# Optimization experiments

Measured on AMD Instinct MI355X. Metric: run time of the kernel, lower is better.

The kernel has to match this reference:

```python
import jax, jax.numpy as jnp
import numpy as np

B, LQ, LK, D = 16, 2048, 2048, 64
TEMPERATURE = 8.0  # sqrt(d_k)


def setup_inputs() -> dict:
    key = jax.random.key(0)
    kq, kk, kv, km = jax.random.split(key, 4)
    q = jax.random.normal(kq, (B, LQ, D), dtype=jnp.float32)
    k = jax.random.normal(kk, (B, LK, D), dtype=jnp.float32)
    v = jax.random.normal(kv, (B, LK, D), dtype=jnp.float32)
    mask = jax.random.randint(km, (B, LQ, LK), 0, 2).astype(jnp.bool_)
    return {"q": q, "k": k, "v": v, "mask": mask}


def reference(q, k, v, mask):
    # attn = bmm(q, k^T) / temperature  -> [B, LQ, LK]
    attn = jnp.einsum("bqd,bkd->bqk", q, k) / TEMPERATURE
    attn = jnp.where(mask, -jnp.inf, attn)
    attn = jax.nn.softmax(attn, axis=2)
    out = jnp.einsum("bqk,bkd->bqd", attn, v)  # [B, LQ, D]
    return out, attn
```

## Files before the change

kernel.cpp:

```cpp
#include <hip/hip_runtime.h>

namespace {
constexpr int kB = 16;
constexpr int kLQ = 2048;
constexpr int kLK = 2048;
constexpr int kD = 64;
constexpr int kQBlk = 16;
constexpr int kStride = 2056;
}

using short8 = __attribute__((ext_vector_type(8))) short;
using f32x4 = __attribute__((ext_vector_type(4))) float;

static __device__ __forceinline__ unsigned short f2bf(float x) {
    unsigned u = __builtin_bit_cast(unsigned, x);
    u += 0x7FFFu + ((u >> 16) & 1u);
    return (unsigned short)(u >> 16);
}
static __device__ __forceinline__ float bf2f(unsigned short s) {
    unsigned u = ((unsigned)s) << 16;
    return __builtin_bit_cast(float, u);
}
static __device__ __forceinline__ short8 cvt8(float4 a, float4 b, float s) {
    return short8{(short)f2bf(a.x*s), (short)f2bf(a.y*s), (short)f2bf(a.z*s), (short)f2bf(a.w*s),
                  (short)f2bf(b.x*s), (short)f2bf(b.y*s), (short)f2bf(b.z*s), (short)f2bf(b.w*s)};
}

__global__ __launch_bounds__(512, 4) void sdpa_v2_kernel(
    const float* __restrict__ qg, const float* __restrict__ kg,
    const float* __restrict__ vg, const void* __restrict__ maskg,
    float* __restrict__ outg, float* __restrict__ attng)
{
    __shared__ unsigned short s_s[kQBlk][kStride];
    __shared__ float s_sum[kQBlk];
    __shared__ int s_flag;

    const int tid = threadIdx.x;
    const int wave = tid >> 6;
    const int lane = tid & 63;
    const int r16 = lane & 15;
    const int g = lane >> 4;

    const int blk = blockIdx.x;
    const int b = blk >> 7;
    const int qrow0 = (blk & 127) * kQBlk;

    if (tid < 64) {
        unsigned w = ((const unsigned*)maskg)[tid];
        unsigned long long bal = __ballot((w & 0xFFFFFF00u) != 0u);
        if (tid == 0) s_flag = (bal != 0ull) ? 1 : 0;
    }
    __syncthreads();
    const bool mask_byte = (s_flag != 0);

    short8 q0, q1;
    {
        const float4* qp = (const float4*)(qg + ((size_t)b * kLQ + qrow0 + r16) * kD);
        float4 x0 = qp[2*g + 0], x1 = qp[2*g + 1];
        float4 x2 = qp[2*g + 8], x3 = qp[2*g + 9];
        q0 = cvt8(x0, x1, 0.125f);
        q1 = cvt8(x2, x3, 0.125f);
    }
    const size_t kbase = (size_t)b * kLK * kD;
    for (int t = wave; t < kLK / 32; t += 8) {
        const int col0 = t * 32;
        const float4* kpA = (const float4*)(kg + kbase + (size_t)(col0 + r16) * kD);
        const float4* kpB = (const float4*)(kg + kbase + (size_t)(col0 + 16 + r16) * kD);
        float4 a0 = kpA[2*g + 0], a1 = kpA[2*g + 1], a2 = kpA[2*g + 8], a3 = kpA[2*g + 9];
        float4 c0 = kpB[2*g + 0], c1 = kpB[2*g + 1], c2 = kpB[2*g + 8], c3 = kpB[2*g + 9];
        short8 kA0 = cvt8(a0, a1, 1.f), kA1 = cvt8(a2, a3, 1.f);
        short8 kB0 = cvt8(c0, c1, 1.f), kB1 = cvt8(c2, c3, 1.f);
        f32x4 accA = {0.f, 0.f, 0.f, 0.f}, accB = {0.f, 0.f, 0.f, 0.f};
        accA = __builtin_amdgcn_mfma_f32_16x16x32_bf16(kA0, q0, accA, 0, 0, 0);
        accA = __builtin_amdgcn_mfma_f32_16x16x32_bf16(kA1, q1, accA, 0, 0, 0);
        accB = __builtin_amdgcn_mfma_f32_16x16x32_bf16(kB0, q0, accB, 0, 0, 0);
        accB = __builtin_amdgcn_mfma_f32_16x16x32_bf16(kB1, q1, accB, 0, 0, 0);
        unsigned long long pA = (unsigned long long)f2bf(accA[0])
                              | ((unsigned long long)f2bf(accA[1]) << 16)
                              | ((unsigned long long)f2bf(accA[2]) << 32)
                              | ((unsigned long long)f2bf(accA[3]) << 48);
        unsigned long long pB = (unsigned long long)f2bf(accB[0])
                              | ((unsigned long long)f2bf(accB[1]) << 16)
                              | ((unsigned long long)f2bf(accB[2]) << 32)
                              | ((unsigned long long)f2bf(accB[3]) << 48);
        *(unsigned long long*)&s_s[r16][col0 + 4*g] = pA;
        *(unsigned long long*)&s_s[r16][col0 + 16 + 4*g] = pB;
    }
    __syncthreads();

    const int rr = tid >> 5;
    const int cc = tid & 31;
    const size_t mrow = ((size_t)b * kLQ + qrow0 + rr) * kLK;
    float sm = 0.f;
    if (mask_byte) {
        const unsigned char* mp = (const unsigned char*)maskg + mrow;
#pragma unroll
        for (int i = 0; i < 8; ++i) {
            const int col = cc * 8 + i * 256;
            const short8 xv = *(const short8*)&s_s[rr][col];
            const unsigned long long mw = *(const unsigned long long*)(mp + col);
#pragma unroll
            for (int j = 0; j < 8; ++j)
                sm += (((mw >> (8*j)) & 0xFFull) == 0) ? __expf(bf2f((unsigned short)xv[j])) : 0.f;
        }
    } else {
        const int* mp = (const int*)maskg + mrow;
#pragma unroll
        for (int i = 0; i < 8; ++i) {
            const int col = cc * 8 + i * 256;
            const short8 xv = *(const short8*)&s_s[rr][col];
            const int4 m0 = *(const int4*)(mp + col);
            const int4 m1 = *(const int4*)(mp + col + 4);
            sm += (m0.x == 0) ? __expf(bf2f((unsigned short)xv[0])) : 0.f;
            sm += (m0.y == 0) ? __expf(bf2f((unsigned short)xv[1])) : 0.f;
            sm += (m0.z == 0) ? __expf(bf2f((unsigned short)xv[2])) : 0.f;
            sm += (m0.w == 0) ? __expf(bf2f((unsigned short)xv[3])) : 0.f;
            sm += (m1.x == 0) ? __expf(bf2f((unsigned short)xv[4])) : 0.f;
            sm += (m1.y == 0) ? __expf(bf2f((unsigned short)xv[5])) : 0.f;
            sm += (m1.z == 0) ? __expf(bf2f((unsigned short)xv[6])) : 0.f;
            sm += (m1.w == 0) ? __expf(bf2f((unsigned short)xv[7])) : 0.f;
        }
    }
#pragma unroll
    for (int off = 16; off >= 1; off >>= 1) sm += __shfl_xor(sm, off, 64);
    if (cc == 0) s_sum[rr] = sm;
    __syncthreads();

    {
        const float rinv = 1.0f / s_sum[rr];
        float* arow = attng + mrow;
        if (mask_byte) {
            const unsigned char* mp = (const unsigned char*)maskg + mrow;
#pragma unroll 4
            for (int i = 0; i < 16; ++i) {
                const int col = cc * 4 + i * 128;
                const unsigned long long sv = *(const unsigned long long*)&s_s[rr][col];
                const unsigned mw = *(const unsigned*)(mp + col);
                float4 a;
                a.x = ((mw & 0x000000FFu) == 0) ? __expf(bf2f((unsigned short)(sv >>  0))) * rinv : 0.f;
                a.y = ((mw & 0x0000FF00u) == 0) ? __expf(bf2f((unsigned short)(sv >> 16))) * rinv : 0.f;
                a.z = ((mw & 0x00FF0000u) == 0) ? __expf(bf2f((unsigned short)(sv >> 32))) * rinv : 0.f;
                a.w = ((mw & 0xFF000000u) == 0) ? __expf(bf2f((unsigned short)(sv >> 48))) * rinv : 0.f;
                *(float4*)(arow + col) = a;
                const unsigned long long nb = (unsigned long long)f2bf(a.x)
                                            | ((unsigned long long)f2bf(a.y) << 16)
                                            | ((unsigned long long)f2bf(a.z) << 32)
                                            | ((unsigned long long)f2bf(a.w) << 48);
                *(unsigned long long*)&s_s[rr][col] = nb;
            }
        } else {
            const int* mp = (const int*)maskg + mrow;
#pragma unroll 4
            for (int i = 0; i < 16; ++i) {
                const int col = cc * 4 + i * 128;
                const unsigned long long sv = *(const unsigned long long*)&s_s[rr][col];
                const int4 mw = *(const int4*)(mp + col);
                float4 a;
                a.x = (mw.x == 0) ? __expf(bf2f((unsigned short)(sv >>  0))) * rinv : 0.f;
                a.y = (mw.y == 0) ? __expf(bf2f((unsigned short)(sv >> 16))) * rinv : 0.f;
                a.z = (mw.z == 0) ? __expf(bf2f((unsigned short)(sv >> 32))) * rinv : 0.f;
                a.w = (mw.w == 0) ? __expf(bf2f((unsigned short)(sv >> 48))) * rinv : 0.f;
                *(float4*)(arow + col) = a;
                const unsigned long long nb = (unsigned long long)f2bf(a.x)
                                            | ((unsigned long long)f2bf(a.y) << 16)
                                            | ((unsigned long long)f2bf(a.z) << 32)
                                            | ((unsigned long long)f2bf(a.w) << 48);
                *(unsigned long long*)&s_s[rr][col] = nb;
            }
        }
    }
    __syncthreads();

    {
        const int d0 = (wave & 3) * 16;
        const int kh = wave >> 2;
        const float* vbase = vg + (size_t)b * kLK * kD + d0 + r16;
        f32x4 acc = {0.f, 0.f, 0.f, 0.f};
#pragma unroll 2
        for (int kt = kh * 32; kt < kh * 32 + 32; ++kt) {
            const int kk0 = kt * 32 + 8 * g;
            const short8 af = *(const short8*)&s_s[r16][kk0];
            float v0 = vbase[(size_t)(kk0 + 0) * kD], v1 = vbase[(size_t)(kk0 + 1) * kD];
            float v2 = vbase[(size_t)(kk0 + 2) * kD], v3 = vbase[(size_t)(kk0 + 3) * kD];
            float v4 = vbase[(size_t)(kk0 + 4) * kD], v5 = vbase[(size_t)(kk0 + 5) * kD];
            float v6 = vbase[(size_t)(kk0 + 6) * kD], v7 = vbase[(size_t)(kk0 + 7) * kD];
            const short8 bv = short8{(short)f2bf(v0), (short)f2bf(v1), (short)f2bf(v2), (short)f2bf(v3),
                                     (short)f2bf(v4), (short)f2bf(v5), (short)f2bf(v6), (short)f2bf(v7)};
            acc = __builtin_amdgcn_mfma_f32_16x16x32_bf16(af, bv, acc, 0, 0, 0);
        }
        __syncthreads();
        float* s_red = (float*)&s_s[0][0];
        if (kh == 1) {
#pragma unroll
            for (int r = 0; r < 4; ++r) s_red[(4*g + r) * 64 + d0 + r16] = acc[r];
        }
        __syncthreads();
        if (kh == 0) {
#pragma unroll
            for (int r = 0; r < 4; ++r) {
                const int m = 4*g + r;
                outg[((size_t)b * kLQ + qrow0 + m) * kD + d0 + r16] = acc[r] + s_red[m * 64 + d0 + r16];
            }
        }
    }
}

extern "C" void kernel_launch(void* const* d_in, const int* in_sizes, int n_in,
                              void* d_out, int out_size, void* d_ws, size_t ws_size,
                              hipStream_t stream) {
    (void)in_sizes; (void)n_in; (void)out_size; (void)d_ws; (void)ws_size;
    const float* q = (const float*)d_in[0];
    const float* k = (const float*)d_in[1];
    const float* v = (const float*)d_in[2];
    const void* mask = d_in[3];
    float* out = (float*)d_out;
    float* attn = out + (size_t)kB * kLQ * kD;
    const dim3 grid(kB * (kLQ / kQBlk));
    sdpa_v2_kernel<<<grid, 512, 0, stream>>>(q, k, v, mask, out, attn);
}
```

Baseline: 260.4 us.

## Fuse masking and exp into QK pass, defer normalization to output

Masking and exponentiation now happen right after the QK MFMAs, and per-wave partial row sums are kept in registers. This removes the separate sum pass, which re-read the mask and recomputed exp. The attention write pass becomes a plain scale of the stored exp values and no longer reads the mask. The PV product uses unnormalized probabilities and scales the output by the reciprocal row sum. A dedicated reduction buffer removes two barriers, at the cost of less coalesced per-row mask reads inside the MFMA loop and slightly different bf16 rounding of the attention values.

```diff
diff --git a/kernel.cpp b/kernel.cpp
--- a/kernel.cpp
+++ b/kernel.cpp
@@ -26,13 +26,14 @@
                   (short)f2bf(b.x*s), (short)f2bf(b.y*s), (short)f2bf(b.z*s), (short)f2bf(b.w*s)};
 }
 
-__global__ __launch_bounds__(512, 4) void sdpa_v2_kernel(
+__global__ __launch_bounds__(512, 4) void sdpa_v3_kernel(
     const float* __restrict__ qg, const float* __restrict__ kg,
     const float* __restrict__ vg, const void* __restrict__ maskg,
     float* __restrict__ outg, float* __restrict__ attng)
 {
     __shared__ unsigned short s_s[kQBlk][kStride];
-    __shared__ float s_sum[kQBlk];
+    __shared__ float s_wsum[8][16];
+    __shared__ float s_red[kQBlk][kD];
     __shared__ int s_flag;
 
     const int tid = threadIdx.x;
@@ -52,6 +53,8 @@
     }
     __syncthreads();
     const bool mask_byte = (s_flag != 0);
+    const unsigned char* mask_u8 = (const unsigned char*)maskg;
+    const int* mask_i32 = (const int*)maskg;
 
     short8 q0, q1;
     {
@@ -62,6 +65,9 @@
         q1 = cvt8(x2, x3, 0.125f);
     }
     const size_t kbase = (size_t)b * kLK * kD;
+    const size_t mrowL = ((size_t)b * kLQ + qrow0 + r16) * (size_t)kLK;
+    float wsum = 0.f;
+
     for (int t = wave; t < kLK / 32; t += 8) {
         const int col0 = t * 32;
         const float4* kpA = (const float4*)(kg + kbase + (size_t)(col0 + r16) * kD);
@@ -75,101 +81,67 @@
         accA = __builtin_amdgcn_mfma_f32_16x16x32_bf16(kA1, q1, accA, 0, 0, 0);
         accB = __builtin_amdgcn_mfma_f32_16x16x32_bf16(kB0, q0, accB, 0, 0, 0);
         accB = __builtin_amdgcn_mfma_f32_16x16x32_bf16(kB1, q1, accB, 0, 0, 0);
-        unsigned long long pA = (unsigned long long)f2bf(accA[0])
-                              | ((unsigned long long)f2bf(accA[1]) << 16)
-                              | ((unsigned long long)f2bf(accA[2]) << 32)
-                              | ((unsigned long long)f2bf(accA[3]) << 48);
-        unsigned long long pB = (unsigned long long)f2bf(accB[0])
-                              | ((unsigned long long)f2bf(accB[1]) << 16)
-                              | ((unsigned long long)f2bf(accB[2]) << 32)
-                              | ((unsigned long long)f2bf(accB[3]) << 48);
-        *(unsigned long long*)&s_s[r16][col0 + 4*g] = pA;
-        *(unsigned long long*)&s_s[r16][col0 + 16 + 4*g] = pB;
+
+        const int cA = col0 + 4*g;
+        const int cB = col0 + 16 + 4*g;
+        float eA[4], eB[4];
+        if (mask_byte) {
+            const unsigned mwA = *(const unsigned*)(mask_u8 + mrowL + cA);
+            const unsigned mwB = *(const unsigned*)(mask_u8 + mrowL + cB);
+#pragma unroll
+            for (int r = 0; r < 4; ++r) {
+                eA[r] = ((mwA >> (8*r)) & 0xFFu) ? 0.f : __expf(accA[r]);
+                eB[r] = ((mwB >> (8*r)) & 0xFFu) ? 0.f : __expf(accB[r]);
+            }
+        } else {
+            const int4 mwA = *(const int4*)(mask_i32 + mrowL + cA);
+            const int4 mwB = *(const int4*)(mask_i32 + mrowL + cB);
+            eA[0] = mwA.x ? 0.f : __expf(accA[0]);
+            eA[1] = mwA.y ? 0.f : __expf(accA[1]);
+            eA[2] = mwA.z ? 0.f : __expf(accA[2]);
+            eA[3] = mwA.w ? 0.f : __expf(accA[3]);
+            eB[0] = mwB.x ? 0.f : __expf(accB[0]);
+            eB[1] = mwB.y ? 0.f : __expf(accB[1]);
+            eB[2] = mwB.z ? 0.f : __expf(accB[2]);
+            eB[3] = mwB.w ? 0.f : __expf(accB[3]);
+        }
+        wsum += (eA[0] + eA[1]) + (eA[2] + eA[3]) + (eB[0] + eB[1]) + (eB[2] + eB[3]);
+        const unsigned long long pA = (unsigned long long)f2bf(eA[0])
+                                    | ((unsigned long long)f2bf(eA[1]) << 16)
+                                    | ((unsigned long long)f2bf(eA[2]) << 32)
+                                    | ((unsigned long long)f2bf(eA[3]) << 48);
+        const unsigned long long pB = (unsigned long long)f2bf(eB[0])
+                                    | ((unsigned long long)f2bf(eB[1]) << 16)
+                                    | ((unsigned long long)f2bf(eB[2]) << 32)
+                                    | ((unsigned long long)f2bf(eB[3]) << 48);
+        *(unsigned long long*)&s_s[r16][cA] = pA;
+        *(unsigned long long*)&s_s[r16][cB] = pB;
     }
-    __syncthreads();
-
-    const int rr = tid >> 5;
-    const int cc = tid & 31;
-    const size_t mrow = ((size_t)b * kLQ + qrow0 + rr) * kLK;
-    float sm = 0.f;
-    if (mask_byte) {
-        const unsigned char* mp = (const unsigned char*)maskg + mrow;
-#pragma unroll
-        for (int i = 0; i < 8; ++i) {
-            const int col = cc * 8 + i * 256;
-            const short8 xv = *(const short8*)&s_s[rr][col];
-            const unsigned long long mw = *(const unsigned long long*)(mp + col);
-#pragma unroll
-            for (int j = 0; j < 8; ++j)
-                sm += (((mw >> (8*j)) & 0xFFull) == 0) ? __expf(bf2f((unsigned short)xv[j])) : 0.f;
-        }
-    } else {
-        const int* mp = (const int*)maskg + mrow;
-#pragma unroll
-        for (int i = 0; i < 8; ++i) {
-            const int col = cc * 8 + i * 256;
-            const short8 xv = *(const short8*)&s_s[rr][col];
-            const int4 m0 = *(const int4*)(mp + col);
-            const int4 m1 = *(const int4*)(mp + col + 4);
-            sm += (m0.x == 0) ? __expf(bf2f((unsigned short)xv[0])) : 0.f;
-            sm += (m0.y == 0) ? __expf(bf2f((unsigned short)xv[1])) : 0.f;
-            sm += (m0.z == 0) ? __expf(bf2f((unsigned short)xv[2])) : 0.f;
-            sm += (m0.w == 0) ? __expf(bf2f((unsigned short)xv[3])) : 0.f;
-            sm += (m1.x == 0) ? __expf(bf2f((unsigned short)xv[4])) : 0.f;
-            sm += (m1.y == 0) ? __expf(bf2f((unsigned short)xv[5])) : 0.f;
-            sm += (m1.z == 0) ? __expf(bf2f((unsigned short)xv[6])) : 0.f;
-            sm += (m1.w == 0) ? __expf(bf2f((unsigned short)xv[7])) : 0.f;
-        }
-    }
-#pragma unroll
-    for (int off = 16; off >= 1; off >>= 1) sm += __shfl_xor(sm, off, 64);
-    if (cc == 0) s_sum[rr] = sm;
+    wsum += __shfl_xor(wsum, 16, 64);
+    wsum += __shfl_xor(wsum, 32, 64);
+    if (g == 0) s_wsum[wave][r16] = wsum;
     __syncthreads();
 
     {
-        const float rinv = 1.0f / s_sum[rr];
-        float* arow = attng + mrow;
-        if (mask_byte) {
-            const unsigned char* mp = (const unsigned char*)maskg + mrow;
+        const int rr = tid >> 5;
+        const int cc = tid & 31;
+        float rsum = 0.f;
+#pragma unroll
+        for (int w = 0; w < 8; ++w) rsum += s_wsum[w][rr];
+        const float rinv = 1.0f / rsum;
+        float* arow = attng + ((size_t)b * kLQ + qrow0 + rr) * kLK;
 #pragma unroll 4
-            for (int i = 0; i < 16; ++i) {
-                const int col = cc * 4 + i * 128;
-                const unsigned long long sv = *(const unsigned long long*)&s_s[rr][col];
-                const unsigned mw = *(const unsigned*)(mp + col);
-                float4 a;
-                a.x = ((mw & 0x000000FFu) == 0) ? __expf(bf2f((unsigned short)(sv >>  0))) * rinv : 0.f;
-                a.y = ((mw & 0x0000FF00u) == 0) ? __expf(bf2f((unsigned short)(sv >> 16))) * rinv : 0.f;
-                a.z = ((mw & 0x00FF0000u) == 0) ? __expf(bf2f((unsigned short)(sv >> 32))) * rinv : 0.f;
-                a.w = ((mw & 0xFF000000u) == 0) ? __expf(bf2f((unsigned short)(sv >> 48))) * rinv : 0.f;
-                *(float4*)(arow + col) = a;
-                const unsigned long long nb = (unsigned long long)f2bf(a.x)
-                                            | ((unsigned long long)f2bf(a.y) << 16)
-                                            | ((unsigned long long)f2bf(a.z) << 32)
-                                            | ((unsigned long long)f2bf(a.w) << 48);
-                *(unsigned long long*)&s_s[rr][col] = nb;
-            }
-        } else {
-            const int* mp = (const int*)maskg + mrow;
-#pragma unroll 4
-            for (int i = 0; i < 16; ++i) {
-                const int col = cc * 4 + i * 128;
-                const unsigned long long sv = *(const unsigned long long*)&s_s[rr][col];
-                const int4 mw = *(const int4*)(mp + col);
-                float4 a;
-                a.x = (mw.x == 0) ? __expf(bf2f((unsigned short)(sv >>  0))) * rinv : 0.f;
-                a.y = (mw.y == 0) ? __expf(bf2f((unsigned short)(sv >> 16))) * rinv : 0.f;
-                a.z = (mw.z == 0) ? __expf(bf2f((unsigned short)(sv >> 32))) * rinv : 0.f;
-                a.w = (mw.w == 0) ? __expf(bf2f((unsigned short)(sv >> 48))) * rinv : 0.f;
-                *(float4*)(arow + col) = a;
-                const unsigned long long nb = (unsigned long long)f2bf(a.x)
-                                            | ((unsigned long long)f2bf(a.y) << 16)
-                                            | ((unsigned long long)f2bf(a.z) << 32)
-                                            | ((unsigned long long)f2bf(a.w) << 48);
-                *(unsigned long long*)&s_s[rr][col] = nb;
-            }
+        for (int i = 0; i < 16; ++i) {
+            const int col = cc * 4 + i * 128;
+            const unsigned long long sv = *(const unsigned long long*)&s_s[rr][col];
+            float4 a;
+            a.x = bf2f((unsigned short)(sv >>  0)) * rinv;
+            a.y = bf2f((unsigned short)(sv >> 16)) * rinv;
+            a.z = bf2f((unsigned short)(sv >> 32)) * rinv;
+            a.w = bf2f((unsigned short)(sv >> 48)) * rinv;
+            *(float4*)(arow + col) = a;
         }
     }
-    __syncthreads();
 
     {
         const int d0 = (wave & 3) * 16;
@@ -188,18 +160,20 @@
                                      (short)f2bf(v4), (short)f2bf(v5), (short)f2bf(v6), (short)f2bf(v7)};
             acc = __builtin_amdgcn_mfma_f32_16x16x32_bf16(af, bv, acc, 0, 0, 0);
         }
-        __syncthreads();
-        float* s_red = (float*)&s_s[0][0];
         if (kh == 1) {
 #pragma unroll
-            for (int r = 0; r < 4; ++r) s_red[(4*g + r) * 64 + d0 + r16] = acc[r];
+            for (int r = 0; r < 4; ++r) s_red[4*g + r][d0 + r16] = acc[r];
         }
         __syncthreads();
         if (kh == 0) {
 #pragma unroll
             for (int r = 0; r < 4; ++r) {
                 const int m = 4*g + r;
-                outg[((size_t)b * kLQ + qrow0 + m) * kD + d0 + r16] = acc[r] + s_red[m * 64 + d0 + r16];
+                float rs = 0.f;
+#pragma unroll
+                for (int w = 0; w < 8; ++w) rs += s_wsum[w][m];
+                outg[((size_t)b * kLQ + qrow0 + m) * kD + d0 + r16] =
+                    (acc[r] + s_red[m][d0 + r16]) * (1.0f / rs);
             }
         }
     }
@@ -216,5 +190,5 @@
     float* out = (float*)d_out;
     float* attn = out + (size_t)kB * kLQ * kD;
     const dim3 grid(kB * (kLQ / kQBlk));
-    sdpa_v2_kernel<<<grid, 512, 0, stream>>>(q, k, v, mask, out, attn);
+    sdpa_v3_kernel<<<grid, 512, 0, stream>>>(q, k, v, mask, out, attn);
 }
```

Measured after the change: 271.4 us. 1.04x slower.
